# Kernel optimization log

Hardware: AMD Instinct MI355X
Metric: run time of the kernel (lower is better)

Reference implementation:

```python
import jax, jax.numpy as jnp
import numpy as np

N_P, N_A, N_T = 20000, 10000, 5000
D_IN, D_OUT = 512, 256
E_P, E_A, E_T = 320000, 160000, 80000


def setup_inputs() -> dict:
    key = jax.random.key(0)
    ks = iter(jax.random.split(key, 64))

    def nrm(shape, scale=1.0):
        return jax.random.normal(next(ks), shape, dtype=jnp.float32) * scale

    def xav(shape):
        # xavier_uniform-like scale (gain 1.414), normal draw is fine for a baseline
        return nrm(shape, 1.414 * (2.0 / (shape[0] + shape[1])) ** 0.5)

    def edges(ne, n_src, n_dst):
        src = jax.random.randint(next(ks), (ne,), 0, n_src, dtype=jnp.int32)
        dst = jax.random.randint(next(ks), (ne,), 0, n_dst, dtype=jnp.int32)
        w = jax.random.uniform(next(ks), (ne,), dtype=jnp.float32) / 16.0  # ~normalized adj values
        return src, dst, w

    d = {}
    d["x_p"] = nrm((N_P, D_IN))
    d["x_a"] = nrm((N_A, D_IN))
    d["x_t"] = nrm((N_T, D_IN))
    d["e_p_a_src"], d["e_p_a_dst"], d["e_p_a_w"] = edges(E_P, N_A, N_P)
    d["e_p_t_src"], d["e_p_t_dst"], d["e_p_t_w"] = edges(E_P, N_T, N_P)
    d["e_a_p_src"], d["e_a_p_dst"], d["e_a_p_w"] = edges(E_A, N_P, N_A)
    d["e_a_t_src"], d["e_a_t_dst"], d["e_a_t_w"] = edges(E_A, N_T, N_A)
    d["e_t_p_src"], d["e_t_p_dst"], d["e_t_p_w"] = edges(E_T, N_P, N_T)
    d["e_t_a_src"], d["e_t_a_dst"], d["e_t_a_w"] = edges(E_T, N_A, N_T)
    # parameters for each target type k: W_proj per neighbor, w_self, w_share, w_att, w_cat, bias
    for k, nbs in (("p", ("a", "t")), ("a", ("p", "t")), ("t", ("p", "a"))):
        for nb in nbs:
            d[f"W_{k}_{nb}"] = xav((D_IN, D_OUT))
        d[f"ws_{k}"] = xav((D_IN, D_OUT))
        d[f"wsh_{k}"] = xav((D_OUT, D_OUT))
        d[f"watt_{k}"] = xav((2 * D_OUT, 1))
        d[f"wcat_{k}"] = xav((2 * D_OUT, D_OUT))
        d[f"b_{k}"] = xav((1, D_OUT))
    return d


def _hete_agg(x_self, w_self, w_share, w_att, w_cat, bias, nb_inputs):
    """nb_inputs: list of (x_nb, W_proj, src, dst, edge_w). Faithful to HeteAggregateLayer."""
    n = x_self.shape[0]
    self_ft = (x_self @ w_self) @ w_share  # [n, d]
    # per-relation: project -> spmm (gather + weighted segment-sum over dst) -> share
    nb_fts = [
        jax.ops.segment_sum((x_nb @ Wp)[src] * ew[:, None], dst, num_segments=n) @ w_share
        for (x_nb, Wp, src, dst, ew) in nb_inputs
    ]
    L = len(nb_fts)
    # e = leaky_relu(cat([cat(nb_ft,0), self_ft.repeat(L,1)],1) @ w_att)  -> [L*n, 1]
    e = jnp.concatenate(
        [jax.nn.leaky_relu(jnp.concatenate([f, self_ft], axis=1) @ w_att) for f in nb_fts],
        axis=0,
    )
    # NOTE: faithful replication of the original `e.view(-1, L)` reshape semantics
    att = jax.nn.softmax(e.reshape(n, L), axis=1)  # [n, L]
    agg = nb_fts[0] * att[:, 0:1]
    for i in range(1, L):
        agg = agg + nb_fts[i] * att[:, i : i + 1]
    return jnp.concatenate([agg, self_ft], axis=1) @ w_cat + bias


def reference(x_p, x_a, x_t,
              e_p_a_src, e_p_a_dst, e_p_a_w, e_p_t_src, e_p_t_dst, e_p_t_w,
              e_a_p_src, e_a_p_dst, e_a_p_w, e_a_t_src, e_a_t_dst, e_a_t_w,
              e_t_p_src, e_t_p_dst, e_t_p_w, e_t_a_src, e_t_a_dst, e_t_a_w,
              W_p_a, W_p_t, ws_p, wsh_p, watt_p, wcat_p, b_p,
              W_a_p, W_a_t, ws_a, wsh_a, watt_a, wcat_a, b_a,
              W_t_p, W_t_a, ws_t, wsh_t, watt_t, wcat_t, b_t):
    out_p = _hete_agg(x_p, ws_p, wsh_p, watt_p, wcat_p, b_p,
                      [(x_a, W_p_a, e_p_a_src, e_p_a_dst, e_p_a_w),
                       (x_t, W_p_t, e_p_t_src, e_p_t_dst, e_p_t_w)])
    out_a = _hete_agg(x_a, ws_a, wsh_a, watt_a, wcat_a, b_a,
                      [(x_p, W_a_p, e_a_p_src, e_a_p_dst, e_a_p_w),
                       (x_t, W_a_t, e_a_t_src, e_a_t_dst, e_a_t_w)])
    out_t = _hete_agg(x_t, ws_t, wsh_t, watt_t, wcat_t, b_t,
                      [(x_p, W_t_p, e_t_p_src, e_t_p_dst, e_t_p_w),
                       (x_a, W_t_a, e_t_a_src, e_t_a_dst, e_t_a_w)])
    return (out_p, out_a, out_t)
```

## Files before the change

### kernel.cpp

```cpp
#include <hip/hip_runtime.h>

namespace {

typedef short s16x8 __attribute__((ext_vector_type(8)));
typedef float f32x4 __attribute__((ext_vector_type(4)));

__device__ __forceinline__ float bf2f(unsigned short u) {
  return __uint_as_float(((unsigned)u) << 16);
}
__device__ __forceinline__ unsigned short f2bf(float f) {
  unsigned u = __float_as_uint(f);
  u += 0x7fffu + ((u >> 16) & 1u);
  return (unsigned short)(u >> 16);
}

typedef __attribute__((address_space(3))) unsigned int lds_u32;
typedef __attribute__((address_space(1))) const unsigned int glob_u32;
__device__ __forceinline__ void gl16(const void* g, void* l) {
  __builtin_amdgcn_global_load_lds((glob_u32*)g, (lds_u32*)l, 16, 0, 0);
}

__global__ __launch_bounds__(256) void cvt_x3(const float* __restrict__ x0,
                                              const float* __restrict__ x1,
                                              const float* __restrict__ x2,
                                              unsigned short* __restrict__ out) {
  size_t i = ((size_t)blockIdx.x * 256 + threadIdx.x) * 8;
  const float* src;
  size_t off;
  if (i < (size_t)20000 * 512) { src = x0; off = i; }
  else if (i < (size_t)30000 * 512) { src = x1; off = i - (size_t)20000 * 512; }
  else { src = x2; off = i - (size_t)30000 * 512; }
  float4 a = *(const float4*)(src + off);
  float4 b = *(const float4*)(src + off + 4);
  s16x8 v;
  v[0] = (short)f2bf(a.x); v[1] = (short)f2bf(a.y);
  v[2] = (short)f2bf(a.z); v[3] = (short)f2bf(a.w);
  v[4] = (short)f2bf(b.x); v[5] = (short)f2bf(b.y);
  v[6] = (short)f2bf(b.z); v[7] = (short)f2bf(b.w);
  *(s16x8*)(out + i) = v;
}

struct Tc6 { const float* src[6]; unsigned short* dst[6]; int R[6]; };
__global__ __launch_bounds__(256) void transpose_cvt(Tc6 a) {
  int mat = blockIdx.z;
  int R = a.R[mat];
  int r0 = blockIdx.y * 32, c0 = blockIdx.x * 32;
  if (r0 >= R) return;
  const float* __restrict__ src = a.src[mat];
  unsigned short* __restrict__ dst = a.dst[mat];
  __shared__ float T[32][33];
  int tx = threadIdx.x & 31, ty = threadIdx.x >> 5;
  #pragma unroll
  for (int j = 0; j < 4; ++j) {
    int r = ty + j * 8;
    T[r][tx] = src[(size_t)(r0 + r) * 256 + c0 + tx];
  }
  __syncthreads();
  #pragma unroll
  for (int j = 0; j < 4; ++j) {
    int c = ty + j * 8;
    dst[(size_t)(c0 + c) * R + r0 + tx] = f2bf(T[tx][c]);
  }
}

struct Comb9 { const unsigned short* A[9]; const float* B[9]; unsigned short* C[9]; };
__global__ __launch_bounds__(256) void combine_mfma(Comb9 g) {
  int z = blockIdx.z;
  const unsigned short* __restrict__ A = g.A[z];
  const float* __restrict__ B = g.B[z];
  unsigned short* __restrict__ C = g.C[z];
  int row0 = blockIdx.y * 128;
  int col0 = blockIdx.x * 128;
  __shared__ unsigned short As[128 * 40];
  __shared__ unsigned short Bs[128 * 40];
  int tid = threadIdx.x, lane = tid & 63, w = tid >> 6;
  int quad = lane >> 4, m16 = lane & 15;
  f32x4 acc[2][8];
  #pragma unroll
  for (int r = 0; r < 2; ++r)
    #pragma unroll
    for (int c = 0; c < 8; ++c) acc[r][c] = (f32x4){0.f, 0.f, 0.f, 0.f};
  for (int k0 = 0; k0 < 256; k0 += 32) {
    #pragma unroll
    for (int i = 0; i < 2; ++i) {
      int ch = tid + i * 256;
      int m = ch >> 2, kk = (ch & 3) * 8;
      *(s16x8*)&As[m * 40 + kk] = *(const s16x8*)(A + (size_t)(row0 + m) * 256 + k0 + kk);
      const float4* bp = (const float4*)(B + (size_t)(col0 + m) * 256 + k0 + kk);
      float4 b0 = bp[0], b1 = bp[1];
      s16x8 bv;
      bv[0] = (short)f2bf(b0.x); bv[1] = (short)f2bf(b0.y);
      bv[2] = (short)f2bf(b0.z); bv[3] = (short)f2bf(b0.w);
      bv[4] = (short)f2bf(b1.x); bv[5] = (short)f2bf(b1.y);
      bv[6] = (short)f2bf(b1.z); bv[7] = (short)f2bf(b1.w);
      *(s16x8*)&Bs[m * 40 + kk] = bv;
    }
    __syncthreads();
    s16x8 af[2], bf[8];
    #pragma unroll
    for (int r = 0; r < 2; ++r)
      af[r] = *(const s16x8*)&As[(w * 32 + r * 16 + m16) * 40 + quad * 8];
    #pragma unroll
    for (int c = 0; c < 8; ++c)
      bf[c] = *(const s16x8*)&Bs[(c * 16 + m16) * 40 + quad * 8];
    #pragma unroll
    for (int r = 0; r < 2; ++r)
      #pragma unroll
      for (int c = 0; c < 8; ++c)
        acc[r][c] = __builtin_amdgcn_mfma_f32_16x16x32_bf16(af[r], bf[c], acc[r][c], 0, 0, 0);
    __syncthreads();
  }
  #pragma unroll
  for (int r = 0; r < 2; ++r)
    #pragma unroll
    for (int i = 0; i < 4; ++i) {
      int row = row0 + w * 32 + r * 16 + quad * 4 + i;
      #pragma unroll
      for (int c = 0; c < 8; ++c)
        C[(size_t)row * 512 + col0 + c * 16 + m16] = f2bf(acc[r][c][i]);
    }
}

#define PROJ_NWG 1656
struct Proj3 { const unsigned short* A[3]; const unsigned short* Bt[3][3];
               unsigned short* C[3][3]; int M[3]; };
__global__ __launch_bounds__(256) void proj_mfma6(Proj3 g) {
  int orig = blockIdx.x;
  int wg = (orig & 7) * 207 + (orig >> 3);
  int s, rem;
  if (wg < 942) { s = 0; rem = wg; }
  else if (wg < 1416) { s = 1; rem = wg - 942; }
  else { s = 2; rem = wg - 1416; }
  int by = rem / 6;
  int bx = rem - by * 6;
  int M = g.M[s];
  int row0 = by * 128;
  if (row0 >= M) return;
  int combo = bx >> 1;
  int col0 = (bx & 1) * 128;
  const unsigned short* __restrict__ A = g.A[s];
  const unsigned short* __restrict__ Bt = g.Bt[s][combo];
  unsigned short* __restrict__ C = g.C[s][combo];
  __shared__ unsigned short As[128 * 32];
  __shared__ unsigned short Bs[128 * 32];
  int tid = threadIdx.x, lane = tid & 63, w = tid >> 6;
  int quad = lane >> 4, m16 = lane & 15;
  int lr = lane >> 2;
  int lk = (((lane & 3) ^ (lr & 3) ^ ((lr >> 2) & 3))) * 8;
  int ar0 = row0 + w * 32 + lr;
  int ar1 = ar0 + 16;
  const unsigned short* a0p = A + (size_t)(ar0 < M ? ar0 : M - 1) * 512 + lk;
  const unsigned short* a1p = A + (size_t)(ar1 < M ? ar1 : M - 1) * 512 + lk;
  const unsigned short* b0p = Bt + (size_t)(col0 + w * 32 + lr) * 512 + lk;
  const unsigned short* b1p = b0p + (size_t)16 * 512;
  unsigned short* as0 = &As[w * 1024];
  unsigned short* as1 = &As[w * 1024 + 512];
  unsigned short* bs0 = &Bs[w * 1024];
  unsigned short* bs1 = &Bs[w * 1024 + 512];
  int wr = (w & 1) * 64, wc = (w >> 1) * 64;
  int sw = ((quad ^ (m16 & 3) ^ ((m16 >> 2) & 3))) * 8;
  f32x4 acc[4][4];
  #pragma unroll
  for (int r = 0; r < 4; ++r)
    #pragma unroll
    for (int c = 0; c < 4; ++c) acc[r][c] = (f32x4){0.f, 0.f, 0.f, 0.f};
  for (int k0 = 0; k0 < 512; k0 += 32) {
    gl16(a0p + k0, as0);
    gl16(a1p + k0, as1);
    gl16(b0p + k0, bs0);
    gl16(b1p + k0, bs1);
    __syncthreads();
    s16x8 af[4], bf[4];
    #pragma unroll
    for (int r = 0; r < 4; ++r)
      af[r] = *(const s16x8*)&As[(wr + r * 16 + m16) * 32 + sw];
    #pragma unroll
    for (int c = 0; c < 4; ++c)
      bf[c] = *(const s16x8*)&Bs[(wc + c * 16 + m16) * 32 + sw];
    #pragma unroll
    for (int r = 0; r < 4; ++r)
      #pragma unroll
      for (int c = 0; c < 4; ++c)
        acc[r][c] = __builtin_amdgcn_mfma_f32_16x16x32_bf16(af[r], bf[c], acc[r][c], 0, 0, 0);
    __syncthreads();
  }
  #pragma unroll
  for (int r = 0; r < 4; ++r)
    #pragma unroll
    for (int i = 0; i < 4; ++i) {
      int row = row0 + wr + r * 16 + quad * 4 + i;
      if (row < M) {
        #pragma unroll
        for (int c = 0; c < 4; ++c)
          C[(size_t)row * 256 + col0 + wc + c * 16 + m16] = f2bf(acc[r][c][i]);
      }
    }
}

struct Edges6 { const int* src[6]; const int* dst[6]; const float* w[6]; int nE[6]; int cbase[6]; };

#define BSH 9
#define NB2 137
#define CAP2 16384
#define NOV 65536
#define CH 1024
#define NPAY 1120000

__global__ __launch_bounds__(256) void bin1(Edges6 ep,
                                            int* __restrict__ bcur, int* __restrict__ ovcnt,
                                            unsigned long long* __restrict__ rec2,
                                            unsigned long long* __restrict__ ovbuf) {
  int rho = blockIdx.y;
  int nE = ep.nE[rho];
  int chunk = blockIdx.x * CH;
  if (chunk >= nE) return;
  int n = nE - chunk; if (n > CH) n = CH;
  const int* __restrict__ srcp = ep.src[rho];
  const int* __restrict__ dstp = ep.dst[rho];
  const float* __restrict__ wp = ep.w[rho];
  int cb = ep.cbase[rho];
  __shared__ int h[256], excl[256], lcur[256], gbase[256], rsv[256];
  __shared__ int wsum[4];
  __shared__ unsigned long long stage[CH];
  int t = threadIdx.x;
  h[t] = 0;
  gbase[t] = 0;
  __syncthreads();
  int gd[4]; unsigned pv[4];
  #pragma unroll
  for (int j = 0; j < 4; ++j) {
    int idx = t + j * 256;
    gd[j] = -1;
    if (idx < n) {
      int e = chunk + idx;
      int g = cb + dstp[e];
      if (g < 0) g = 0;
      if (g > 69999) g = 69999;
      gd[j] = g;
      pv[j] = (((unsigned)f2bf(wp[e])) << 16) | ((unsigned)srcp[e] & 0x7fffu);
      atomicAdd(&h[g >> BSH], 1);
    }
  }
  __syncthreads();
  int hv = h[t];
  int lane = t & 63, wv = t >> 6;
  int v = hv;
  #pragma unroll
  for (int off = 1; off < 64; off <<= 1) {
    int u = __shfl_up(v, off, 64);
    if (lane >= off) v += u;
  }
  if (lane == 63) wsum[wv] = v;
  __syncthreads();
  int add = 0;
  #pragma unroll
  for (int k = 0; k < 3; ++k)
    if (k < wv) add += wsum[k];
  v += add;
  int ex = v - hv;
  excl[t] = ex;
  lcur[t] = ex;
  int rv = 0;
  if (t < NB2 && hv > 0) {
    rv = (hv + 7) & ~7;
    gbase[t] = atomicAdd(&bcur[t], rv);
  }
  rsv[t] = rv;
  __syncthreads();
  #pragma unroll
  for (int j = 0; j < 4; ++j) {
    if (gd[j] >= 0) {
      int b = gd[j] >> BSH;
      int slot = atomicAdd(&lcur[b], 1);
      if (slot >= 0 && slot < CH)
        stage[slot] = ((unsigned long long)(unsigned)gd[j] << 32) | pv[j];
    }
  }
  __syncthreads();
  for (int s = t; s < n; s += 256) {
    int lo = 0, hi = NB2 - 1;
    while (lo < hi) {
      int mid = (lo + hi + 1) >> 1;
      if (excl[mid] <= s) lo = mid; else hi = mid - 1;
    }
    int b = lo;
    int gp = gbase[b] + (s - excl[b]);
    if (gp >= 0 && gp < CAP2) rec2[(size_t)b * CAP2 + gp] = stage[s];
    else { int op = atomicAdd(ovcnt, 1); ovbuf[op & (NOV - 1)] = stage[s]; }
  }
  for (int b = t; b < NB2; b += 256) {
    int hvb = h[b], rvb = rsv[b], gb = gbase[b];
    for (int k = hvb; k < rvb; ++k) {
      int gp = gb + k;
      if (gp >= 0 && gp < CAP2) rec2[(size_t)b * CAP2 + gp] = 0xFFFFFFFFFFFFFFFFull;
    }
  }
}

__global__ __launch_bounds__(256) void cnt2(const int* __restrict__ bcur,
                                            const unsigned long long* __restrict__ rec2,
                                            const int* __restrict__ ovcnt,
                                            const unsigned long long* __restrict__ ovbuf,
                                            int* __restrict__ counts) {
  int b = blockIdx.x;
  __shared__ int c[512];
  int t = threadIdx.x;
  c[t] = 0; c[t + 256] = 0;
  __syncthreads();
  int nrec = bcur[b];
  nrec = nrec < CAP2 ? nrec : CAP2;
  const unsigned long long* rp = rec2 + (size_t)b * CAP2;
  for (int i = t; i < nrec; i += 256) {
    int gd = (int)(rp[i] >> 32);
    if (gd >= 0) atomicAdd(&c[gd & 511], 1);
  }
  int ovn = *ovcnt;
  ovn = ovn < NOV ? ovn : NOV;
  for (int i = t; i < ovn; i += 256) {
    int gd = (int)(ovbuf[i] >> 32);
    if (gd >= 0 && (gd >> BSH) == b) atomicAdd(&c[gd & 511], 1);
  }
  __syncthreads();
  int g0 = (b << BSH) + t;
  if (g0 < 70000) counts[g0] = c[t];
  int g1 = g0 + 256;
  if (g1 < 70000) counts[g1] = c[t + 256];
}

__global__ __launch_bounds__(256) void scan1(const int* __restrict__ cnt, int* __restrict__ out,
                                             int* __restrict__ part, int len) {
  __shared__ int sh[256];
  int base = blockIdx.x * 2048 + threadIdx.x * 8;
  int v[8];
  int s = 0;
  #pragma unroll
  for (int j = 0; j < 8; ++j) {
    int i = base + j;
    int x = (i < len) ? cnt[i] : 0;
    v[j] = s;
    s += x;
  }
  sh[threadIdx.x] = s;
  __syncthreads();
  for (int off = 1; off < 256; off <<= 1) {
    int t = (threadIdx.x >= off) ? sh[threadIdx.x - off] : 0;
    __syncthreads();
    sh[threadIdx.x] += t;
    __syncthreads();
  }
  int texcl = sh[threadIdx.x] - s;
  #pragma unroll
  for (int j = 0; j < 8; ++j) {
    int i = base + j;
    if (i < len) out[i] = texcl + v[j];
  }
  if (threadIdx.x == 255) part[blockIdx.x] = sh[255];
}

__global__ void scan2(int* __restrict__ part, int nb, int* __restrict__ total_out) {
  __shared__ int sh[64];
  int t = threadIdx.x;
  int v = (t < nb) ? part[t] : 0;
  sh[t] = v;
  __syncthreads();
  for (int off = 1; off < 64; off <<= 1) {
    int x = (t >= off) ? sh[t - off] : 0;
    __syncthreads();
    sh[t] += x;
    __syncthreads();
  }
  if (t < nb) part[t] = sh[t] - v;
  if (t == 63) *total_out = sh[63];
}

__global__ __launch_bounds__(256) void scan3(int* __restrict__ offs,
                                             const int* __restrict__ part, int len) {
  int i = blockIdx.x * 256 + threadIdx.x;
  if (i >= len) return;
  offs[i] += part[i >> 11];
}

__global__ __launch_bounds__(512) void fine2(const int* __restrict__ offs,
                                             const int* __restrict__ bcur,
                                             const unsigned long long* __restrict__ rec2,
                                             const int* __restrict__ ovcnt,
                                             const unsigned long long* __restrict__ ovbuf,
                                             unsigned int* __restrict__ pay) {
  int b = blockIdx.x;
  __shared__ int cur[512];
  int t = threadIdx.x;
  {
    int gd = (b << BSH) + t;
    cur[t] = (gd < 70000) ? offs[gd] : 0;
  }
  __syncthreads();
  int nrec = bcur[b];
  nrec = nrec < CAP2 ? nrec : CAP2;
  const unsigned long long* rp = rec2 + (size_t)b * CAP2;
  for (int i = t; i < nrec; i += 512) {
    unsigned long long r = rp[i];
    int gd = (int)(r >> 32);
    if (gd < 0) continue;
    int pos = atomicAdd(&cur[gd & 511], 1);
    if (pos >= 0 && pos < NPAY) pay[pos] = (unsigned)r;
  }
  int ovn = *ovcnt;
  ovn = ovn < NOV ? ovn : NOV;
  for (int i = t; i < ovn; i += 512) {
    unsigned long long r = ovbuf[i];
    int gd = (int)(r >> 32);
    if (gd >= 0 && (gd >> BSH) == b) {
      int pos = atomicAdd(&cur[gd & 511], 1);
      if (pos >= 0 && pos < NPAY) pay[pos] = (unsigned)r;
    }
  }
}

#define GAT_NWG 17500
struct Gather6 { const unsigned short* proj[6]; unsigned short* out[6]; int cb[6]; int n[6]; };
__global__ __launch_bounds__(256) void gather_all(Gather6 g, const int* __restrict__ offs,
                                                  const unsigned int* __restrict__ pay) {
  int orig = blockIdx.x;
  int xcd = orig & 7, idx = orig >> 3;
  int wg = (xcd < 4 ? xcd * 2188 : 4 * 2188 + (xcd - 4) * 2187) + idx;
  int rho, base;
  if (wg < 5000) { rho = 0; base = 0; }
  else if (wg < 10000) { rho = 1; base = 5000; }
  else if (wg < 12500) { rho = 2; base = 10000; }
  else if (wg < 15000) { rho = 3; base = 12500; }
  else if (wg < 16250) { rho = 4; base = 15000; }
  else { rho = 5; base = 16250; }
  int n = g.n[rho];
  int d = (wg - base) * 4 + (threadIdx.x >> 6);
  if (d >= n) return;
  int lane = threadIdx.x & 63, half = lane >> 5, l32 = lane & 31;
  const unsigned short* __restrict__ proj = g.proj[rho];
  const int* of = offs + g.cb[rho];
  int s0 = of[d], s1 = of[d + 1];
  float acc[8] = {};
  int e = s0 + half;
  for (; e + 6 < s1; e += 8) {
    unsigned int u0 = pay[e], u1 = pay[e + 2], u2 = pay[e + 4], u3 = pay[e + 6];
    float wt0 = bf2f((unsigned short)(u0 >> 16));
    float wt1 = bf2f((unsigned short)(u1 >> 16));
    float wt2 = bf2f((unsigned short)(u2 >> 16));
    float wt3 = bf2f((unsigned short)(u3 >> 16));
    s16x8 v0 = *(const s16x8*)(proj + (size_t)(u0 & 0xffffu) * 256 + l32 * 8);
    s16x8 v1 = *(const s16x8*)(proj + (size_t)(u1 & 0xffffu) * 256 + l32 * 8);
    s16x8 v2 = *(const s16x8*)(proj + (size_t)(u2 & 0xffffu) * 256 + l32 * 8);
    s16x8 v3 = *(const s16x8*)(proj + (size_t)(u3 & 0xffffu) * 256 + l32 * 8);
    #pragma unroll
    for (int j = 0; j < 8; ++j) {
      acc[j] = fmaf(bf2f((unsigned short)v0[j]), wt0, acc[j]);
      acc[j] = fmaf(bf2f((unsigned short)v1[j]), wt1, acc[j]);
      acc[j] = fmaf(bf2f((unsigned short)v2[j]), wt2, acc[j]);
      acc[j] = fmaf(bf2f((unsigned short)v3[j]), wt3, acc[j]);
    }
  }
  for (; e < s1; e += 2) {
    unsigned int u = pay[e];
    float wt = bf2f((unsigned short)(u >> 16));
    s16x8 v = *(const s16x8*)(proj + (size_t)(u & 0xffffu) * 256 + l32 * 8);
    #pragma unroll
    for (int j = 0; j < 8; ++j) acc[j] = fmaf(bf2f((unsigned short)v[j]), wt, acc[j]);
  }
  #pragma unroll
  for (int j = 0; j < 8; ++j) acc[j] += __shfl(acc[j], lane ^ 32, 64);
  if (half == 0) {
    s16x8 o;
    #pragma unroll
    for (int j = 0; j < 8; ++j) o[j] = (short)f2bf(acc[j]);
    *(s16x8*)(g.out[rho] + (size_t)d * 256 + l32 * 8) = o;
  }
}

struct Att3 { const unsigned short* nb[3]; const unsigned short* self[3];
              const float* watt[3]; float* att[3]; int n[3]; };
__global__ __launch_bounds__(256) void e_att3(Att3 g) {
  int z = blockIdx.z;
  int n = g.n[z];
  int wv = threadIdx.x >> 6;
  int idx = blockIdx.x * 4 + wv;
  int lane = threadIdx.x & 63;
  __shared__ float ev[4];
  float sum = 0.f;
  if (idx < 2 * n) {
    int i = idx < n ? idx : idx - n;
    ushort4 v  = *(const ushort4*)(g.nb[z] + (size_t)idx * 256 + (lane << 2));
    ushort4 sv = *(const ushort4*)(g.self[z] + (size_t)i * 256 + (lane << 2));
    float4 wa = *(const float4*)(g.watt[z] + (lane << 2));
    float4 wb = *(const float4*)(g.watt[z] + 256 + (lane << 2));
    sum = bf2f(v.x) * wa.x + bf2f(v.y) * wa.y + bf2f(v.z) * wa.z + bf2f(v.w) * wa.w +
          bf2f(sv.x) * wb.x + bf2f(sv.y) * wb.y + bf2f(sv.z) * wb.z + bf2f(sv.w) * wb.w;
    #pragma unroll
    for (int off = 32; off > 0; off >>= 1) sum += __shfl_down(sum, off, 64);
  }
  if (lane == 0) ev[wv] = sum;
  __syncthreads();
  if (threadIdx.x < 2) {
    int base = blockIdx.x * 4 + threadIdx.x * 2;
    if (base < 2 * n) {
      float f0 = ev[threadIdx.x * 2], f1 = ev[threadIdx.x * 2 + 1];
      f0 = f0 > 0.f ? f0 : 0.01f * f0;
      f1 = f1 > 0.f ? f1 : 0.01f * f1;
      float m = fmaxf(f0, f1);
      float a = expf(f0 - m), b = expf(f1 - m);
      float inv = 1.f / (a + b);
      g.att[z][base] = a * inv;
      g.att[z][base + 1] = b * inv;
    }
  }
}

struct Fin3 { const unsigned short* nb[3]; const unsigned short* self[3]; const float* att[3];
              const unsigned short* Wt[3]; const float* bias[3]; float* out[3]; int M[3]; };
__global__ __launch_bounds__(256, 3) void final_mfma3(Fin3 g) {
  int z = blockIdx.z;
  int M = g.M[z];
  int row0 = blockIdx.y * 64;
  if (row0 >= M) return;
  const unsigned short* __restrict__ nbft = g.nb[z];
  const unsigned short* __restrict__ selfb = g.self[z];
  const float* __restrict__ att = g.att[z];
  const unsigned short* __restrict__ Wt = g.Wt[z];
  __shared__ unsigned short As[64 * 40];
  __shared__ unsigned short Bs[256 * 40];
  int tid = threadIdx.x, lane = tid & 63, w = tid >> 6;
  int quad = lane >> 4, m16 = lane & 15;
  int am = tid >> 2, akk = (tid & 3) * 8;
  int gr = row0 + am;
  float a0 = 0.f, a1 = 0.f;
  if (gr < M) { a0 = att[2 * gr]; a1 = att[2 * gr + 1]; }
  f32x4 acc[4][4];
  #pragma unroll
  for (int r = 0; r < 4; ++r)
    #pragma unroll
    for (int c = 0; c < 4; ++c) acc[r][c] = (f32x4){0.f, 0.f, 0.f, 0.f};

  s16x8 pu0 = {}, pu1 = {};
  s16x8 pb[4];

  auto loadA = [&](int k0) {
    int kg = k0 + akk;
    if (gr < M) {
      if (kg < 256) {
        pu0 = *(const s16x8*)(nbft + (size_t)gr * 256 + kg);
        pu1 = *(const s16x8*)(nbft + ((size_t)M + gr) * 256 + kg);
      } else {
        pu0 = *(const s16x8*)(selfb + (size_t)gr * 256 + (kg - 256));
      }
    }
  };
  auto loadB = [&](int k0) {
    #pragma unroll
    for (int i = 0; i < 4; ++i) {
      int ch = tid + i * 256;
      int m = ch >> 2, kk = (ch & 3) * 8;
      pb[i] = *(const s16x8*)(Wt + (size_t)m * 512 + k0 + kk);
    }
  };
  auto storeLDS = [&](int k0) {
    int kg = k0 + akk;
    s16x8 v = {};
    if (gr < M) {
      if (kg < 256) {
        #pragma unroll
        for (int j = 0; j < 8; ++j)
          v[j] = (short)f2bf(fmaf(a0, bf2f((unsigned short)pu0[j]),
                                  a1 * bf2f((unsigned short)pu1[j])));
      } else {
        v = pu0;
      }
    }
    *(s16x8*)&As[am * 40 + akk] = v;
    #pragma unroll
    for (int i = 0; i < 4; ++i) {
      int ch = tid + i * 256;
      int m = ch >> 2, kk = (ch & 3) * 8;
      *(s16x8*)&Bs[m * 40 + kk] = pb[i];
    }
  };

  loadA(0); loadB(0); storeLDS(0);
  __syncthreads();
  for (int k0 = 0; k0 < 512; k0 += 32) {
    int kn = k0 + 32;
    if (kn < 512) { loadA(kn); loadB(kn); }
    s16x8 af[4], bf[4];
    #pragma unroll
    for (int r = 0; r < 4; ++r)
      af[r] = *(const s16x8*)&As[(r * 16 + m16) * 40 + quad * 8];
    #pragma unroll
    for (int c = 0; c < 4; ++c)
      bf[c] = *(const s16x8*)&Bs[(w * 64 + c * 16 + m16) * 40 + quad * 8];
    #pragma unroll
    for (int r = 0; r < 4; ++r)
      #pragma unroll
      for (int c = 0; c < 4; ++c)
        acc[r][c] = __builtin_amdgcn_mfma_f32_16x16x32_bf16(af[r], bf[c], acc[r][c], 0, 0, 0);
    __syncthreads();
    if (kn < 512) {
      storeLDS(kn);
      __syncthreads();
    }
  }
  const float* __restrict__ bias = g.bias[z];
  float* __restrict__ out = g.out[z];
  #pragma unroll
  for (int r = 0; r < 4; ++r)
    #pragma unroll
    for (int i = 0; i < 4; ++i) {
      int row = row0 + r * 16 + quad * 4 + i;
      if (row < M) {
        #pragma unroll
        for (int c = 0; c < 4; ++c) {
          int col = w * 64 + c * 16 + m16;
          out[(size_t)row * 256 + col] = acc[r][c][i] + bias[col];
        }
      }
    }
}

}

extern "C" void kernel_launch(void* const* d_in, const int* in_sizes, int n_in,
                              void* d_out, int out_size, void* d_ws, size_t ws_size,
                              hipStream_t stream) {
  (void)in_sizes; (void)n_in; (void)out_size; (void)ws_size;
  const float* x[3] = {(const float*)d_in[0], (const float*)d_in[1], (const float*)d_in[2]};

  char* p = (char*)d_ws;
  unsigned short* projfull = (unsigned short*)p;  p += (size_t)105000 * 256 * 2;
  unsigned short* nbft = (unsigned short*)p;      p += (size_t)70000 * 256 * 2;
  unsigned short* wcatbt = (unsigned short*)p;    p += (size_t)3 * 256 * 512 * 2;
  int* offs = (int*)p;                            p += (size_t)70004 * 4;
  int* counts = (int*)p;                          p += (size_t)70000 * 4;
  int* bcur = (int*)p;                            p += 160 * 4;
  int* ovcnt = (int*)p;                           p += 16;
  int* part = (int*)p;                            p += 256;
  float* att_buf = (float*)p;                     p += (size_t)70000 * 4;
  unsigned int* csr_pay = (unsigned int*)p;       p += (size_t)1120000 * 4;
  unsigned short* wshT = nbft;
  unsigned short* Wcbt = (unsigned short*)((char*)nbft + 393216);
  unsigned long long* rec2 = (unsigned long long*)projfull;
  unsigned long long* ovbuf = rec2 + (size_t)NB2 * CAP2;
  unsigned short* xb = (unsigned short*)d_out;

  const int n_of[3] = {20000, 10000, 5000};
  const int nbt[3][2] = {{1, 2}, {0, 2}, {0, 1}};
  const int ebase[3][2] = {{3, 6}, {9, 12}, {15, 18}};
  const int nE3[3] = {320000, 160000, 80000};
  const size_t out_off[3] = {0, (size_t)20000 * 256, (size_t)30000 * 256};
  const int tstart[3] = {0, 15000, 40000};
  const int selfoff[3] = {70000, 90000, 100000};
  const int nboff[3] = {0, 40000, 60000};
  const int xboff[3] = {0, 20000, 30000};

  cvt_x3<<<dim3(8750), 256, 0, stream>>>(x[0], x[1], x[2], xb);

  Tc6 tc;
  for (int t = 0; t < 3; ++t) {
    tc.src[t] = (const float*)d_in[21 + t * 7 + 3];
    tc.dst[t] = wshT + (size_t)t * 256 * 256;
    tc.R[t] = 256;
    tc.src[3 + t] = (const float*)d_in[21 + t * 7 + 5];
    tc.dst[3 + t] = wcatbt + (size_t)t * 256 * 512;
    tc.R[3 + t] = 512;
  }
  transpose_cvt<<<dim3(8, 16, 6), 256, 0, stream>>>(tc);

  Comb9 c9;
  for (int t = 0; t < 3; ++t) {
    int wb = 21 + t * 7;
    for (int j = 0; j < 3; ++j) {
      int combo = t * 3 + j;
      c9.A[combo] = wshT + (size_t)t * 256 * 256;
      c9.B[combo] = (const float*)d_in[wb + j];
      c9.C[combo] = Wcbt + (size_t)combo * 256 * 512;
    }
  }
  combine_mfma<<<dim3(4, 2, 9), 256, 0, stream>>>(c9);

  Edges6 ep;
  const int cbase[6] = {0, 20000, 40000, 50000, 60000, 65000};
  for (int t = 0; t < 3; ++t)
    for (int r = 0; r < 2; ++r) {
      int rho = t * 2 + r, eb = ebase[t][r];
      ep.src[rho] = (const int*)d_in[eb];
      ep.dst[rho] = (const int*)d_in[eb + 1];
      ep.w[rho] = (const float*)d_in[eb + 2];
      ep.nE[rho] = nE3[t];
      ep.cbase[rho] = cbase[rho];
    }
  hipMemsetAsync(bcur, 0, 160 * 4 + 16, stream);
  bin1<<<dim3(313, 6), 256, 0, stream>>>(ep, bcur, ovcnt, rec2, ovbuf);
  cnt2<<<NB2, 256, 0, stream>>>(bcur, rec2, ovcnt, ovbuf, counts);
  scan1<<<35, 256, 0, stream>>>(counts, offs, part, 70000);
  scan2<<<1, 64, 0, stream>>>(part, 35, offs + 70000);
  scan3<<<274, 256, 0, stream>>>(offs, part, 70000);
  fine2<<<NB2, 512, 0, stream>>>(offs, bcur, rec2, ovcnt, ovbuf, csr_pay);

  Proj3 pj;
  {
    int cnum[3] = {0, 0, 0};
    for (int t = 0; t < 3; ++t) {
      int m0 = n_of[nbt[t][0]];
      for (int j = 0; j < 3; ++j) {
        int s = (j == 2) ? t : nbt[t][j];
        unsigned short* dst =
            (j == 0) ? projfull + (size_t)tstart[t] * 256
          : (j == 1) ? projfull + (size_t)(tstart[t] + m0) * 256
                     : projfull + (size_t)selfoff[t] * 256;
        int c = cnum[s]++;
        pj.Bt[s][c] = Wcbt + (size_t)(t * 3 + j) * 256 * 512;
        pj.C[s][c] = dst;
      }
    }
    for (int s = 0; s < 3; ++s) {
      pj.A[s] = xb + (size_t)xboff[s] * 512;
      pj.M[s] = n_of[s];
    }
  }
  proj_mfma6<<<dim3(PROJ_NWG), 256, 0, stream>>>(pj);

  Gather6 gt;
  for (int t = 0; t < 3; ++t) {
    int m0 = n_of[nbt[t][0]];
    for (int r = 0; r < 2; ++r) {
      int rho = t * 2 + r;
      gt.proj[rho] = projfull + (size_t)(tstart[t] + (r ? m0 : 0)) * 256;
      gt.out[rho] = nbft + (size_t)(nboff[t] + r * n_of[t]) * 256;
      gt.cb[rho] = cbase[rho];
      gt.n[rho] = n_of[t];
    }
  }
  gather_all<<<dim3(GAT_NWG), 256, 0, stream>>>(gt, offs, csr_pay);

  Att3 at;
  for (int t = 0; t < 3; ++t) {
    at.nb[t] = nbft + (size_t)nboff[t] * 256;
    at.self[t] = projfull + (size_t)selfoff[t] * 256;
    at.watt[t] = (const float*)d_in[21 + t * 7 + 4];
    at.att[t] = att_buf + nboff[t];
    at.n[t] = n_of[t];
  }
  e_att3<<<dim3(10000, 1, 3), 256, 0, stream>>>(at);

  Fin3 fn;
  for (int t = 0; t < 3; ++t) {
    fn.nb[t] = nbft + (size_t)nboff[t] * 256;
    fn.self[t] = projfull + (size_t)selfoff[t] * 256;
    fn.att[t] = att_buf + nboff[t];
    fn.Wt[t] = wcatbt + (size_t)t * 256 * 512;
    fn.bias[t] = (const float*)d_in[21 + t * 7 + 6];
    fn.out[t] = (float*)d_out + out_off[t];
    fn.M[t] = n_of[t];
  }
  final_mfma3<<<dim3(1, 313, 3), 256, 0, stream>>>(fn);
}
```

Baseline: 396.5 us.

## Fuse attention score dot products into the gather epilogue and split the softmax out

The neighbour half of the attention logit is now computed inside the gather kernel from its fp32 accumulators, right after the aggregation. The self half is precomputed once per node by a new small kernel. A lightweight kernel then applies leaky-relu and the pairwise softmax, replacing the old attention kernel that re-read every aggregated neighbour row and self row from memory. This removes a full pass over the aggregated neighbour buffer. In exchange it adds a launch, a small cross-lane reduction in the gather tail, and reuse of the counts and attention buffers as scratch space.

```diff
diff --git a/kernel.cpp b/kernel.cpp
--- a/kernel.cpp
+++ b/kernel.cpp
@@ -416,8 +416,28 @@
   }
 }
 
+struct Sd3 { const unsigned short* self[3]; const float* watt[3]; float* sdot[3]; };
+__global__ __launch_bounds__(256) void selfdot3(Sd3 g) {
+  int r = blockIdx.x * 4 + (threadIdx.x >> 6);
+  int t, base;
+  if (r < 20000) { t = 0; base = 0; }
+  else if (r < 30000) { t = 1; base = 20000; }
+  else if (r < 35000) { t = 2; base = 30000; }
+  else return;
+  int lane = threadIdx.x & 63;
+  int d = r - base;
+  ushort4 v = *(const ushort4*)(g.self[t] + (size_t)d * 256 + (lane << 2));
+  float4 wb = *(const float4*)(g.watt[t] + 256 + (lane << 2));
+  float s = bf2f(v.x) * wb.x + bf2f(v.y) * wb.y + bf2f(v.z) * wb.z + bf2f(v.w) * wb.w;
+  #pragma unroll
+  for (int off = 32; off > 0; off >>= 1) s += __shfl_down(s, off, 64);
+  if (lane == 0) g.sdot[t][d] = s;
+}
+
 #define GAT_NWG 17500
-struct Gather6 { const unsigned short* proj[6]; unsigned short* out[6]; int cb[6]; int n[6]; };
+struct Gather6 { const unsigned short* proj[6]; unsigned short* out[6];
+                 const float* watt[6]; const float* sdot[6]; float* esc[6];
+                 int cb[6]; int n[6]; };
 __global__ __launch_bounds__(256) void gather_all(Gather6 g, const int* __restrict__ offs,
                                                   const unsigned int* __restrict__ pay) {
   int orig = blockIdx.x;
@@ -472,44 +492,32 @@
     for (int j = 0; j < 8; ++j) o[j] = (short)f2bf(acc[j]);
     *(s16x8*)(g.out[rho] + (size_t)d * 256 + l32 * 8) = o;
   }
-}
-
-struct Att3 { const unsigned short* nb[3]; const unsigned short* self[3];
-              const float* watt[3]; float* att[3]; int n[3]; };
-__global__ __launch_bounds__(256) void e_att3(Att3 g) {
-  int z = blockIdx.z;
-  int n = g.n[z];
-  int wv = threadIdx.x >> 6;
-  int idx = blockIdx.x * 4 + wv;
-  int lane = threadIdx.x & 63;
-  __shared__ float ev[4];
-  float sum = 0.f;
-  if (idx < 2 * n) {
-    int i = idx < n ? idx : idx - n;
-    ushort4 v  = *(const ushort4*)(g.nb[z] + (size_t)idx * 256 + (lane << 2));
-    ushort4 sv = *(const ushort4*)(g.self[z] + (size_t)i * 256 + (lane << 2));
-    float4 wa = *(const float4*)(g.watt[z] + (lane << 2));
-    float4 wb = *(const float4*)(g.watt[z] + 256 + (lane << 2));
-    sum = bf2f(v.x) * wa.x + bf2f(v.y) * wa.y + bf2f(v.z) * wa.z + bf2f(v.w) * wa.w +
-          bf2f(sv.x) * wb.x + bf2f(sv.y) * wb.y + bf2f(sv.z) * wb.z + bf2f(sv.w) * wb.w;
-    #pragma unroll
-    for (int off = 32; off > 0; off >>= 1) sum += __shfl_down(sum, off, 64);
-  }
-  if (lane == 0) ev[wv] = sum;
-  __syncthreads();
-  if (threadIdx.x < 2) {
-    int base = blockIdx.x * 4 + threadIdx.x * 2;
-    if (base < 2 * n) {
-      float f0 = ev[threadIdx.x * 2], f1 = ev[threadIdx.x * 2 + 1];
-      f0 = f0 > 0.f ? f0 : 0.01f * f0;
-      f1 = f1 > 0.f ? f1 : 0.01f * f1;
-      float m = fmaxf(f0, f1);
-      float a = expf(f0 - m), b = expf(f1 - m);
-      float inv = 1.f / (a + b);
-      g.att[z][base] = a * inv;
-      g.att[z][base + 1] = b * inv;
-    }
-  }
+  float4 wa0 = *(const float4*)(g.watt[rho] + (l32 << 3));
+  float4 wa1 = *(const float4*)(g.watt[rho] + (l32 << 3) + 4);
+  float sc = acc[0] * wa0.x + acc[1] * wa0.y + acc[2] * wa0.z + acc[3] * wa0.w +
+             acc[4] * wa1.x + acc[5] * wa1.y + acc[6] * wa1.z + acc[7] * wa1.w;
+  #pragma unroll
+  for (int off = 16; off > 0; off >>= 1) sc += __shfl_xor(sc, off, 64);
+  if (lane == 0) g.esc[rho][d] = sc + g.sdot[rho][d];
+}
+
+struct Es3 { const float* esc[3]; float* att[3]; int n[3]; };
+__global__ __launch_bounds__(256) void e_soft(Es3 g) {
+  int i = blockIdx.x * 256 + threadIdx.x;
+  int t, base;
+  if (i < 20000) { t = 0; base = 0; }
+  else if (i < 30000) { t = 1; base = 20000; }
+  else if (i < 35000) { t = 2; base = 30000; }
+  else return;
+  int d = i - base;
+  float f0 = g.esc[t][2 * d], f1 = g.esc[t][2 * d + 1];
+  f0 = f0 > 0.f ? f0 : 0.01f * f0;
+  f1 = f1 > 0.f ? f1 : 0.01f * f1;
+  float m = fmaxf(f0, f1);
+  float a = expf(f0 - m), b = expf(f1 - m);
+  float inv = 1.f / (a + b);
+  g.att[t][2 * d] = a * inv;
+  g.att[t][2 * d + 1] = b * inv;
 }
 
 struct Fin3 { const unsigned short* nb[3]; const unsigned short* self[3]; const float* att[3];
@@ -644,6 +652,7 @@
   unsigned short* Wcbt = (unsigned short*)((char*)nbft + 393216);
   unsigned long long* rec2 = (unsigned long long*)projfull;
   unsigned long long* ovbuf = rec2 + (size_t)NB2 * CAP2;
+  float* esc_buf = (float*)counts;
   unsigned short* xb = (unsigned short*)d_out;
 
   const int n_of[3] = {20000, 10000, 5000};
@@ -655,6 +664,7 @@
   const int selfoff[3] = {70000, 90000, 100000};
   const int nboff[3] = {0, 40000, 60000};
   const int xboff[3] = {0, 20000, 30000};
+  const int sdotoff[3] = {0, 20000, 30000};
 
   cvt_x3<<<dim3(8750), 256, 0, stream>>>(x[0], x[1], x[2], xb);
 
@@ -723,6 +733,14 @@
   }
   proj_mfma6<<<dim3(PROJ_NWG), 256, 0, stream>>>(pj);
 
+  Sd3 sd;
+  for (int t = 0; t < 3; ++t) {
+    sd.self[t] = projfull + (size_t)selfoff[t] * 256;
+    sd.watt[t] = (const float*)d_in[21 + t * 7 + 4];
+    sd.sdot[t] = att_buf + sdotoff[t];
+  }
+  selfdot3<<<dim3(8750), 256, 0, stream>>>(sd);
+
   Gather6 gt;
   for (int t = 0; t < 3; ++t) {
     int m0 = n_of[nbt[t][0]];
@@ -730,21 +748,22 @@
       int rho = t * 2 + r;
       gt.proj[rho] = projfull + (size_t)(tstart[t] + (r ? m0 : 0)) * 256;
       gt.out[rho] = nbft + (size_t)(nboff[t] + r * n_of[t]) * 256;
+      gt.watt[rho] = (const float*)d_in[21 + t * 7 + 4];
+      gt.sdot[rho] = att_buf + sdotoff[t];
+      gt.esc[rho] = esc_buf + nboff[t] + r * n_of[t];
       gt.cb[rho] = cbase[rho];
       gt.n[rho] = n_of[t];
     }
   }
   gather_all<<<dim3(GAT_NWG), 256, 0, stream>>>(gt, offs, csr_pay);
 
-  Att3 at;
+  Es3 es;
   for (int t = 0; t < 3; ++t) {
-    at.nb[t] = nbft + (size_t)nboff[t] * 256;
-    at.self[t] = projfull + (size_t)selfoff[t] * 256;
-    at.watt[t] = (const float*)d_in[21 + t * 7 + 4];
-    at.att[t] = att_buf + nboff[t];
-    at.n[t] = n_of[t];
-  }
-  e_att3<<<dim3(10000, 1, 3), 256, 0, stream>>>(at);
+    es.esc[t] = esc_buf + nboff[t];
+    es.att[t] = att_buf + nboff[t];
+    es.n[t] = n_of[t];
+  }
+  e_soft<<<dim3(137), 256, 0, stream>>>(es);
 
   Fin3 fn;
   for (int t = 0; t < 3; ++t) {
```

Result: no change. 394.7 us (median of 2 runs) (-0.4%).
